# Kernel optimization log

Measured on AMD Instinct MI355X. Metric: run time of the kernel, lower is better.

Reference implementation:

```python
import jax, jax.numpy as jnp
import numpy as np

B, S, DEC, ENC, ATTN = 64, 1024, 1024, 1024, 1024

def setup_inputs() -> dict:
    key = jax.random.key(0)
    k1, k2, k3, k4, k5 = jax.random.split(key, 5)
    hidden = jax.random.normal(k1, (B, DEC), dtype=jnp.float32)
    encoder_outputs = jax.random.normal(k2, (B, S, ENC), dtype=jnp.float32)
    # nn.Linear(dec+enc -> attn_dim): weight [attn, dec+enc], bias [attn]
    fan_in = DEC + ENC
    bound = 1.0 / np.sqrt(fan_in)
    W_attn = jax.random.uniform(k3, (ATTN, fan_in), dtype=jnp.float32, minval=-bound, maxval=bound)
    b_attn = jax.random.uniform(k4, (ATTN,), dtype=jnp.float32, minval=-bound, maxval=bound)
    # v = torch.rand(attn_dim) -> uniform [0,1)
    v = jax.random.uniform(k5, (ATTN,), dtype=jnp.float32)
    return {"hidden": hidden, "encoder_outputs": encoder_outputs,
            "W_attn": W_attn, "b_attn": b_attn, "v": v}

def reference(hidden, encoder_outputs, W_attn, b_attn, v):
    # hidden: [B, DEC], encoder_outputs: [B, S, ENC]
    b, s, _ = encoder_outputs.shape
    h = jnp.broadcast_to(hidden[:, None, :], (b, s, hidden.shape[-1]))
    combined = jnp.concatenate([h, encoder_outputs], axis=-1)        # [B, S, DEC+ENC]
    energy = jnp.tanh(jnp.einsum('bsf,af->bsa', combined, W_attn) + b_attn)  # [B, S, ATTN]
    scores = jnp.einsum('bsa,a->bs', energy, v)                      # [B, S]
    attn_weights = jax.nn.softmax(scores, axis=1)                    # [B, S]
    context = jnp.einsum('bs,bse->be', attn_weights, encoder_outputs)[:, None, :]  # [B, 1, ENC]
    return context
```

## Files before the change

### kernel.cpp

```cpp
#include <hip/hip_runtime.h>
#include <hip/hip_bf16.h>
#include <stdint.h>

#define NB 64
#define NS 1024
#define NE 1024
#define NA 1024
#define NF 2048
#define LDP 144

typedef __attribute__((ext_vector_type(8))) short   short8;
typedef __attribute__((ext_vector_type(4))) short   short4v;
typedef __attribute__((ext_vector_type(4))) float   f32x4;
typedef __attribute__((ext_vector_type(8))) __bf16  bf16x8;

__device__ __forceinline__ unsigned short f2bf(float x) {
  union { float f; unsigned u; } v; v.f = x;
  unsigned r = v.u + 0x7fffu + ((v.u >> 16) & 1u);
  return (unsigned short)(r >> 16);
}
__device__ __forceinline__ float bf2f(unsigned short h) {
  union { unsigned u; float f; } v; v.u = ((unsigned)h) << 16;
  return v.f;
}
__device__ __forceinline__ float tanh_fast(float x) {
  float e = __expf(2.0f * x);
  return 1.0f - __fdividef(2.0f, e + 1.0f);
}
__device__ __forceinline__ short8 pack8(float4 a, float4 b) {
  short8 h;
  h[0]=(short)f2bf(a.x); h[1]=(short)f2bf(a.y); h[2]=(short)f2bf(a.z); h[3]=(short)f2bf(a.w);
  h[4]=(short)f2bf(b.x); h[5]=(short)f2bf(b.y); h[6]=(short)f2bf(b.z); h[7]=(short)f2bf(b.w);
  return h;
}
__device__ __forceinline__ void gload_lds16(const void* g, void* l) {
  __builtin_amdgcn_global_load_lds((const __attribute__((address_space(1))) void*)g,
                                   (__attribute__((address_space(3))) void*)l, 16, 0, 0);
}

__global__ __launch_bounds__(256) void k_zero(float4* __restrict__ p, int n4) {
  int i = blockIdx.x * 256 + threadIdx.x;
  if (i < n4) { float4 z; z.x = z.y = z.z = z.w = 0.f; p[i] = z; }
}

__global__ __launch_bounds__(256) void k_conv_enc(const float4* __restrict__ src,
                                                  short8* __restrict__ dst, int n8) {
  int i = blockIdx.x * 256 + threadIdx.x;
  const int stride = gridDim.x * 256;
  for (; i < n8; i += stride) {
    float4 a = src[2 * i], b = src[2 * i + 1];
    dst[i] = pack8(a, b);
  }
}

__global__ __launch_bounds__(256) void k_conv_w(const float* __restrict__ W, short8* __restrict__ dst) {
  const int id = blockIdx.x * 256 + threadIdx.x;
  const int a = id >> 7, ku = id & 127;
  const float* s = W + (size_t)a * NF + 1024 + ku * 8;
  float4 x = *(const float4*)s;
  float4 y = *(const float4*)(s + 4);
  dst[id] = pack8(x, y);
}

__global__ __launch_bounds__(256) void k_u(const float* __restrict__ hidden,
                                           const float* __restrict__ W,
                                           const float* __restrict__ bias,
                                           float* __restrict__ u) {
  const int l = threadIdx.x & 63;
  const int w = threadIdx.x >> 6;
  const int a = (blockIdx.x >> 1) * 4 + w;
  const int bh = blockIdx.x & 1;
  const float* wrow = W + (size_t)a * NF;
  float4 wv[4];
  #pragma unroll
  for (int i = 0; i < 4; ++i) wv[i] = *(const float4*)(wrow + l * 4 + i * 256);
  const float ba = bias[a];
  for (int b = bh * 32; b < bh * 32 + 32; ++b) {
    const float* hrow = hidden + b * 1024;
    float s = 0.f;
    #pragma unroll
    for (int i = 0; i < 4; ++i) {
      float4 hv = *(const float4*)(hrow + l * 4 + i * 256);
      s += wv[i].x * hv.x + wv[i].y * hv.y + wv[i].z * hv.z + wv[i].w * hv.w;
    }
    #pragma unroll
    for (int m = 1; m < 64; m <<= 1) s += __shfl_xor(s, m);
    if (l == 0) u[b * NA + a] = s + ba;
  }
}

__global__ __launch_bounds__(512, 2) void k_main256(const unsigned short* __restrict__ Ab,
                                                    const unsigned short* __restrict__ Bb,
                                                    const float* __restrict__ u_,
                                                    const float* __restrict__ v_,
                                                    float* __restrict__ scores) {
  __shared__ __align__(16) char smem[2 * 65536];

  const int tid = threadIdx.x;
  const int l = tid & 63;
  const int w = tid >> 6;
  const int wr = w >> 2, wc = w & 3;
  const int d = blockIdx.x;
  const int xcd = d & 7, q = d >> 3;
  const int rt = xcd * 32 + (q >> 2);
  const int ct = q & 3;
  const int b = rt >> 2;
  const int lh = l >> 4, l15 = l & 15, l7 = l & 7;

  const int ssk = ((tid & 7) ^ ((tid >> 3) & 7)) * 8;
  const unsigned short* aS = Ab + (size_t)(rt * 256 + (tid >> 3)) * NE + ssk;
  const unsigned short* bS = Bb + (size_t)(ct * 256 + (tid >> 3)) * NE + ssk;
  const int wdst = w * 1024;

  f32x4 acc[8][4] = {};

#define STAGE256(tt) do { \
    char* dst_ = smem + (((tt) & 1) << 16); \
    const unsigned short* a_ = aS + (size_t)(tt) * 64; \
    const unsigned short* b_ = bS + (size_t)(tt) * 64; \
    gload_lds16(a_,                    dst_ + wdst); \
    gload_lds16(a_ + (size_t) 64 * NE, dst_ +  64 * 128 + wdst); \
    gload_lds16(a_ + (size_t)128 * NE, dst_ + 128 * 128 + wdst); \
    gload_lds16(a_ + (size_t)192 * NE, dst_ + 192 * 128 + wdst); \
    gload_lds16(b_,                    dst_ + 32768 + wdst); \
    gload_lds16(b_ + (size_t) 64 * NE, dst_ + 32768 +  64 * 128 + wdst); \
    gload_lds16(b_ + (size_t)128 * NE, dst_ + 32768 + 128 * 128 + wdst); \
    gload_lds16(b_ + (size_t)192 * NE, dst_ + 32768 + 192 * 128 + wdst); } while (0)

  STAGE256(0);

  for (int t = 0; t < 16; ++t) {
    asm volatile("s_waitcnt vmcnt(0)" ::: "memory");
    asm volatile("s_barrier" ::: "memory");
    if (t < 15) STAGE256(t + 1);

    const char* As = smem + ((t & 1) << 16);
    const char* Bs = As + 32768;

    bf16x8 areg[8][2];
    #pragma unroll
    for (int rf = 0; rf < 8; ++rf)
      #pragma unroll
      for (int kh = 0; kh < 2; ++kh)
        areg[rf][kh] = *(const bf16x8*)(As + (wr * 128 + rf * 16 + l15) * 128
                                           + (((kh * 4 + lh) ^ l7) << 4));
    #pragma unroll
    for (int cfh = 0; cfh < 2; ++cfh) {
      bf16x8 breg[2][2];
      #pragma unroll
      for (int c2 = 0; c2 < 2; ++c2)
        #pragma unroll
        for (int kh = 0; kh < 2; ++kh)
          breg[c2][kh] = *(const bf16x8*)(Bs + (wc * 64 + (cfh * 2 + c2) * 16 + l15) * 128
                                             + (((kh * 4 + lh) ^ l7) << 4));
      __builtin_amdgcn_s_setprio(1);
      #pragma unroll
      for (int rf = 0; rf < 8; ++rf)
        #pragma unroll
        for (int c2 = 0; c2 < 2; ++c2)
          #pragma unroll
          for (int kh = 0; kh < 2; ++kh)
            acc[rf][cfh * 2 + c2] = __builtin_amdgcn_mfma_f32_16x16x32_bf16(
                areg[rf][kh], breg[c2][kh], acc[rf][cfh * 2 + c2], 0, 0, 0);
      __builtin_amdgcn_s_setprio(0);
    }
  }
#undef STAGE256

  const int colb = ct * 256 + wc * 64 + l15;
  float uv[4], vv[4];
  #pragma unroll
  for (int cf = 0; cf < 4; ++cf) {
    const int c = colb + cf * 16;
    uv[cf] = u_[b * NA + c];
    vv[cf] = v_[c];
  }
  #pragma unroll
  for (int rf = 0; rf < 8; ++rf) {
    #pragma unroll
    for (int reg = 0; reg < 4; ++reg) {
      float sacc = 0.f;
      #pragma unroll
      for (int cf = 0; cf < 4; ++cf)
        sacc += tanh_fast(acc[rf][cf][reg] + uv[cf]) * vv[cf];
      sacc += __shfl_xor(sacc, 1);
      sacc += __shfl_xor(sacc, 2);
      sacc += __shfl_xor(sacc, 4);
      sacc += __shfl_xor(sacc, 8);
      if (l15 == 0) {
        const int m = rt * 256 + wr * 128 + rf * 16 + lh * 4 + reg;
        atomicAdd(&scores[m], sacc);
      }
    }
  }
}

template <int ACONV, int BCONV>
__global__ __launch_bounds__(256) void k_main_rs(const void* __restrict__ Asrc,
                                                 const void* __restrict__ Bsrc,
                                                 const float* __restrict__ u_,
                                                 const float* __restrict__ v_,
                                                 float* __restrict__ scores) {
  __shared__ __align__(16) char smemf[2 * 128 * LDP];
  char* As = smemf;
  char* Bs = smemf + 128 * LDP;
  const int tid = threadIdx.x;
  const int l = tid & 63;
  const int w = tid >> 6;
  const int wr = w >> 1, wc = w & 1;
  const int d = blockIdx.x;
  const int rt = (d & 7) * 64 + (d >> 6);
  const int ct = (d >> 3) & 7;
  const int b = rt >> 3;
  const int l7 = l & 7, lh = l >> 4, l15 = l & 15;
  const int srow = w * 8 + (l >> 3);
  f32x4 acc[4][4] = {};
  for (int kt = 0; kt < 16; ++kt) {
    const int k0 = kt * 64;
    __syncthreads();
    #pragma unroll
    for (int r = 0; r < 4; ++r) {
      const int row = r * 32 + srow;
      short8 val;
      if constexpr (ACONV) {
        const float* s = (const float*)Asrc + (size_t)(rt * 128 + row) * NE + k0 + l7 * 8;
        val = pack8(*(const float4*)s, *(const float4*)(s + 4));
      } else {
        val = *(const short8*)((const unsigned short*)Asrc + (size_t)(rt * 128 + row) * NE + k0 + l7 * 8);
      }
      *(short8*)(As + row * LDP + l7 * 16) = val;
    }
    #pragma unroll
    for (int r = 0; r < 4; ++r) {
      const int row = r * 32 + srow;
      short8 val;
      if constexpr (BCONV) {
        const float* s = (const float*)Bsrc + (size_t)(ct * 128 + row) * NF + 1024 + k0 + l7 * 8;
        val = pack8(*(const float4*)s, *(const float4*)(s + 4));
      } else {
        val = *(const short8*)((const unsigned short*)Bsrc + (size_t)(ct * 128 + row) * NE + k0 + l7 * 8);
      }
      *(short8*)(Bs + row * LDP + l7 * 16) = val;
    }
    __syncthreads();
    #pragma unroll
    for (int ks = 0; ks < 2; ++ks) {
      bf16x8 af[4], bfr[4];
      const int ku = (ks * 4 + lh) * 16;
      #pragma unroll
      for (int f = 0; f < 4; ++f) {
        af[f]  = *(const bf16x8*)(As + (wr * 64 + f * 16 + l15) * LDP + ku);
        bfr[f] = *(const bf16x8*)(Bs + (wc * 64 + f * 16 + l15) * LDP + ku);
      }
      #pragma unroll
      for (int i = 0; i < 4; ++i)
        #pragma unroll
        for (int jj = 0; jj < 4; ++jj)
          acc[i][jj] = __builtin_amdgcn_mfma_f32_16x16x32_bf16(af[i], bfr[jj], acc[i][jj], 0, 0, 0);
    }
  }
  const int colb = ct * 128 + wc * 64 + l15;
  float uv[4], vv[4];
  #pragma unroll
  for (int jj = 0; jj < 4; ++jj) {
    const int c = colb + jj * 16;
    uv[jj] = u_[b * NA + c];
    vv[jj] = v_[c];
  }
  #pragma unroll
  for (int i = 0; i < 4; ++i) {
    #pragma unroll
    for (int reg = 0; reg < 4; ++reg) {
      float sacc = 0.f;
      #pragma unroll
      for (int jj = 0; jj < 4; ++jj)
        sacc += tanh_fast(acc[i][jj][reg] + uv[jj]) * vv[jj];
      sacc += __shfl_xor(sacc, 1);
      sacc += __shfl_xor(sacc, 2);
      sacc += __shfl_xor(sacc, 4);
      sacc += __shfl_xor(sacc, 8);
      if (l15 == 0) {
        const int m = rt * 128 + wr * 64 + i * 16 + lh * 4 + reg;
        atomicAdd(&scores[m], sacc);
      }
    }
  }
}

__global__ __launch_bounds__(256) void k_softmax(float* __restrict__ sc) {
  const int b = blockIdx.x, t = threadIdx.x;
  float4 x = *(float4*)(sc + b * NS + t * 4);
  float mx = fmaxf(fmaxf(x.x, x.y), fmaxf(x.z, x.w));
  #pragma unroll
  for (int m = 1; m < 64; m <<= 1) mx = fmaxf(mx, __shfl_xor(mx, m));
  __shared__ float rmax[4], rsum[4];
  if ((t & 63) == 0) rmax[t >> 6] = mx;
  __syncthreads();
  mx = fmaxf(fmaxf(rmax[0], rmax[1]), fmaxf(rmax[2], rmax[3]));
  float e0 = __expf(x.x - mx), e1 = __expf(x.y - mx);
  float e2 = __expf(x.z - mx), e3 = __expf(x.w - mx);
  float sm = e0 + e1 + e2 + e3;
  #pragma unroll
  for (int m = 1; m < 64; m <<= 1) sm += __shfl_xor(sm, m);
  if ((t & 63) == 0) rsum[t >> 6] = sm;
  __syncthreads();
  sm = rsum[0] + rsum[1] + rsum[2] + rsum[3];
  const float inv = 1.0f / sm;
  float4 o; o.x = e0 * inv; o.y = e1 * inv; o.z = e2 * inv; o.w = e3 * inv;
  *(float4*)(sc + b * NS + t * 4) = o;
}

template <int CONV>
__global__ __launch_bounds__(256) void k_ctx(const void* __restrict__ encsrc,
                                             const float* __restrict__ wgt,
                                             float* __restrict__ ctx) {
  const int b = blockIdx.x >> 4, scn = blockIdx.x & 15;
  const int t = threadIdx.x;
  float a0 = 0.f, a1 = 0.f, a2 = 0.f, a3 = 0.f;
  for (int s = scn * 64; s < scn * 64 + 64; ++s) {
    const float wv = wgt[b * NS + s];
    const size_t base = ((size_t)(b * NS + s)) * NE + t * 4;
    if constexpr (CONV) {
      float4 x = *((const float4*)((const float*)encsrc + base));
      a0 += wv * x.x; a1 += wv * x.y; a2 += wv * x.z; a3 += wv * x.w;
    } else {
      short4v hv = *(const short4v*)((const unsigned short*)encsrc + base);
      a0 += wv * bf2f((unsigned short)hv[0]);
      a1 += wv * bf2f((unsigned short)hv[1]);
      a2 += wv * bf2f((unsigned short)hv[2]);
      a3 += wv * bf2f((unsigned short)hv[3]);
    }
  }
  float* c = ctx + b * NE + t * 4;
  atomicAdd(c + 0, a0); atomicAdd(c + 1, a1);
  atomicAdd(c + 2, a2); atomicAdd(c + 3, a3);
}

__global__ __launch_bounds__(256) void k_out(const float* __restrict__ ctx,
                                             float* __restrict__ out) {
  const int i = blockIdx.x * 256 + threadIdx.x;
  float4 x = *(const float4*)(ctx + i * 4);
  *(float4*)(out + i * 4) = x;
}

extern "C" void kernel_launch(void* const* d_in, const int* in_sizes, int n_in,
                              void* d_out, int out_size, void* d_ws, size_t ws_size,
                              hipStream_t stream) {
  const float* hidden = (const float*)d_in[0];
  const float* enc    = (const float*)d_in[1];
  const float* W      = (const float*)d_in[2];
  const float* bias   = (const float*)d_in[3];
  const float* v      = (const float*)d_in[4];
  (void)in_sizes; (void)n_in; (void)out_size;

  char* ws = (char*)d_ws;
  const size_t T0 = (4ull << 20) + (128ull << 20);
  const size_t T1 = (3ull << 20);
  const int tier = (ws_size >= T0) ? 0 : ((ws_size >= T1) ? 1 : 2);

  unsigned short* Wb   = (unsigned short*)ws;
  unsigned short* encb = (unsigned short*)(ws + (4ull << 20));
  float* u_  = (tier < 2) ? (float*)(ws + (2ull << 20)) : (float*)ws;
  float* sc  = u_ + NB * NA;
  float* ctx = sc + NB * NS;

  k_u<<<512, 256, 0, stream>>>(hidden, W, bias, u_);
  k_zero<<<128, 256, 0, stream>>>((float4*)sc, (NB * NS + NB * NE) / 4);

  if (tier == 0) {
    k_conv_w<<<512, 256, 0, stream>>>(W, (short8*)Wb);
    k_conv_enc<<<2048, 256, 0, stream>>>((const float4*)enc, (short8*)encb, NB * NS * NE / 8);
    k_main256<<<1024, 512, 0, stream>>>(encb, Wb, u_, v, sc);
  } else if (tier == 1) {
    k_conv_w<<<512, 256, 0, stream>>>(W, (short8*)Wb);
    k_main_rs<1, 0><<<4096, 256, 0, stream>>>(enc, Wb, u_, v, sc);
  } else {
    k_main_rs<1, 1><<<4096, 256, 0, stream>>>(enc, W, u_, v, sc);
  }

  k_softmax<<<64, 256, 0, stream>>>(sc);
  if (tier == 0) k_ctx<0><<<1024, 256, 0, stream>>>(encb, sc, ctx);
  else           k_ctx<1><<<1024, 256, 0, stream>>>(enc, sc, ctx);
  k_out<<<64, 256, 0, stream>>>(ctx, (float*)d_out);
}
```

Baseline: 281.5 us.

## Interleave global-to-LDS prefetch in four chunks across MFMA phases

The main GEMM loop now splits each k-step into four MFMA quadrants and issues a quarter of the next tile's global-to-LDS loads before each quadrant, with barriers between phases. Previously all eight loads were issued at once at the top of the loop. Spreading the loads is meant to smooth memory traffic and overlap it with matrix math. It adds three extra barriers per iteration and changes register use, since A fragments are now held as two halves and all B fragments are loaded up front.

```diff
diff --git a/kernel.cpp b/kernel.cpp
--- a/kernel.cpp
+++ b/kernel.cpp
@@ -114,58 +114,94 @@
 
   f32x4 acc[8][4] = {};
 
-#define STAGE256(tt) do { \
+#define STG2(tt, p) do { \
     char* dst_ = smem + (((tt) & 1) << 16); \
-    const unsigned short* a_ = aS + (size_t)(tt) * 64; \
-    const unsigned short* b_ = bS + (size_t)(tt) * 64; \
-    gload_lds16(a_,                    dst_ + wdst); \
-    gload_lds16(a_ + (size_t) 64 * NE, dst_ +  64 * 128 + wdst); \
-    gload_lds16(a_ + (size_t)128 * NE, dst_ + 128 * 128 + wdst); \
-    gload_lds16(a_ + (size_t)192 * NE, dst_ + 192 * 128 + wdst); \
-    gload_lds16(b_,                    dst_ + 32768 + wdst); \
-    gload_lds16(b_ + (size_t) 64 * NE, dst_ + 32768 +  64 * 128 + wdst); \
-    gload_lds16(b_ + (size_t)128 * NE, dst_ + 32768 + 128 * 128 + wdst); \
-    gload_lds16(b_ + (size_t)192 * NE, dst_ + 32768 + 192 * 128 + wdst); } while (0)
-
-  STAGE256(0);
+    if ((p) < 2) { \
+      const unsigned short* a_ = aS + (size_t)(tt) * 64 + (size_t)(p) * 128 * NE; \
+      gload_lds16(a_,                   dst_ + (p) * 128 * 128 + wdst); \
+      gload_lds16(a_ + (size_t)64 * NE, dst_ + (p) * 128 * 128 + 64 * 128 + wdst); \
+    } else { \
+      const unsigned short* b_ = bS + (size_t)(tt) * 64 + (size_t)((p) - 2) * 128 * NE; \
+      gload_lds16(b_,                   dst_ + 32768 + ((p) - 2) * 128 * 128 + wdst); \
+      gload_lds16(b_ + (size_t)64 * NE, dst_ + 32768 + ((p) - 2) * 128 * 128 + 64 * 128 + wdst); \
+    } } while (0)
+
+  STG2(0, 0); STG2(0, 1); STG2(0, 2); STG2(0, 3);
 
   for (int t = 0; t < 16; ++t) {
     asm volatile("s_waitcnt vmcnt(0)" ::: "memory");
     asm volatile("s_barrier" ::: "memory");
-    if (t < 15) STAGE256(t + 1);
 
     const char* As = smem + ((t & 1) << 16);
     const char* Bs = As + 32768;
-
-    bf16x8 areg[8][2];
-    #pragma unroll
-    for (int rf = 0; rf < 8; ++rf)
+    bf16x8 areg[4][2], breg[4][2];
+
+    if (t < 15) STG2(t + 1, 0);
+    #pragma unroll
+    for (int rf = 0; rf < 4; ++rf)
       #pragma unroll
       for (int kh = 0; kh < 2; ++kh)
         areg[rf][kh] = *(const bf16x8*)(As + (wr * 128 + rf * 16 + l15) * 128
                                            + (((kh * 4 + lh) ^ l7) << 4));
     #pragma unroll
-    for (int cfh = 0; cfh < 2; ++cfh) {
-      bf16x8 breg[2][2];
-      #pragma unroll
-      for (int c2 = 0; c2 < 2; ++c2)
+    for (int cf = 0; cf < 4; ++cf)
+      #pragma unroll
+      for (int kh = 0; kh < 2; ++kh)
+        breg[cf][kh] = *(const bf16x8*)(Bs + (wc * 64 + cf * 16 + l15) * 128
+                                           + (((kh * 4 + lh) ^ l7) << 4));
+    __builtin_amdgcn_s_setprio(1);
+    #pragma unroll
+    for (int rf = 0; rf < 4; ++rf)
+      #pragma unroll
+      for (int cf = 0; cf < 2; ++cf)
         #pragma unroll
         for (int kh = 0; kh < 2; ++kh)
-          breg[c2][kh] = *(const bf16x8*)(Bs + (wc * 64 + (cfh * 2 + c2) * 16 + l15) * 128
-                                             + (((kh * 4 + lh) ^ l7) << 4));
-      __builtin_amdgcn_s_setprio(1);
-      #pragma unroll
-      for (int rf = 0; rf < 8; ++rf)
+          acc[rf][cf] = __builtin_amdgcn_mfma_f32_16x16x32_bf16(areg[rf][kh], breg[cf][kh], acc[rf][cf], 0, 0, 0);
+    __builtin_amdgcn_s_setprio(0);
+    asm volatile("s_barrier" ::: "memory");
+
+    if (t < 15) STG2(t + 1, 1);
+    __builtin_amdgcn_s_setprio(1);
+    #pragma unroll
+    for (int rf = 0; rf < 4; ++rf)
+      #pragma unroll
+      for (int cf = 2; cf < 4; ++cf)
         #pragma unroll
-        for (int c2 = 0; c2 < 2; ++c2)
-          #pragma unroll
-          for (int kh = 0; kh < 2; ++kh)
-            acc[rf][cfh * 2 + c2] = __builtin_amdgcn_mfma_f32_16x16x32_bf16(
-                areg[rf][kh], breg[c2][kh], acc[rf][cfh * 2 + c2], 0, 0, 0);
-      __builtin_amdgcn_s_setprio(0);
-    }
-  }
-#undef STAGE256
+        for (int kh = 0; kh < 2; ++kh)
+          acc[rf][cf] = __builtin_amdgcn_mfma_f32_16x16x32_bf16(areg[rf][kh], breg[cf][kh], acc[rf][cf], 0, 0, 0);
+    __builtin_amdgcn_s_setprio(0);
+    asm volatile("s_barrier" ::: "memory");
+
+    if (t < 15) STG2(t + 1, 2);
+    #pragma unroll
+    for (int rf = 0; rf < 4; ++rf)
+      #pragma unroll
+      for (int kh = 0; kh < 2; ++kh)
+        areg[rf][kh] = *(const bf16x8*)(As + (wr * 128 + (4 + rf) * 16 + l15) * 128
+                                           + (((kh * 4 + lh) ^ l7) << 4));
+    __builtin_amdgcn_s_setprio(1);
+    #pragma unroll
+    for (int rf = 0; rf < 4; ++rf)
+      #pragma unroll
+      for (int cf = 0; cf < 2; ++cf)
+        #pragma unroll
+        for (int kh = 0; kh < 2; ++kh)
+          acc[4 + rf][cf] = __builtin_amdgcn_mfma_f32_16x16x32_bf16(areg[rf][kh], breg[cf][kh], acc[4 + rf][cf], 0, 0, 0);
+    __builtin_amdgcn_s_setprio(0);
+    asm volatile("s_barrier" ::: "memory");
+
+    if (t < 15) STG2(t + 1, 3);
+    __builtin_amdgcn_s_setprio(1);
+    #pragma unroll
+    for (int rf = 0; rf < 4; ++rf)
+      #pragma unroll
+      for (int cf = 2; cf < 4; ++cf)
+        #pragma unroll
+        for (int kh = 0; kh < 2; ++kh)
+          acc[4 + rf][cf] = __builtin_amdgcn_mfma_f32_16x16x32_bf16(areg[rf][kh], breg[cf][kh], acc[4 + rf][cf], 0, 0, 0);
+    __builtin_amdgcn_s_setprio(0);
+  }
+#undef STG2
 
   const int colb = ct * 256 + wc * 64 + l15;
   float uv[4], vv[4];
```

New measurement: 284.7 us. No clear change (+1.1%).
